# Kernel tuning notes

Measured on AMD Instinct MI355X. Metric: run time of the kernel, lower is better.

## Reference

```python
import jax, jax.numpy as jnp
import numpy as np

B, N, D, H = 8, 1024, 512, 8
DK = D // H  # key_dim == val_dim == 64
LN_EPS = 1e-5


def setup_inputs() -> dict:
    key = jax.random.key(0)
    ks = jax.random.split(key, 16)
    stdv = 1.0 / np.sqrt(D)
    u = lambda k, shape, s: jax.random.uniform(k, shape, jnp.float32, -s, s)
    inp = {
        'q': jax.random.normal(ks[0], (B, N, D), jnp.float32),
        'mask': jax.random.uniform(ks[1], (B, N, N)) < 0.1,  # True = masked out
        # eps1 is torch.zeros in the source (never re-initialized); use small
        'eps1': jax.random.normal(ks[2], (D, D), jnp.float32) * 0.03,
        # 3 MLP layers, stacked on leading axis. Linear: y = x @ W.T + b
        'U_w': u(ks[3], (3, D, D), stdv), 'U_b': u(ks[4], (3, D), stdv),
        'V_w': u(ks[5], (3, D, D), stdv), 'V_b': u(ks[6], (3, D), stdv),
        'ln_g': jnp.ones((3, D), jnp.float32), 'ln_b': jnp.zeros((3, D), jnp.float32),
        'W_query': u(ks[7], (H, D, DK), 1.0 / np.sqrt(DK)),
        'W_key':   u(ks[8], (H, D, DK), 1.0 / np.sqrt(DK)),
        'W_val':   u(ks[9], (H, D, DK), 1.0 / np.sqrt(DK)),
        'W_out':   u(ks[10], (H, DK, D), stdv),
    }
    return inp


def _layer_norm(x, g, b):
    mu = jnp.mean(x, axis=-1, keepdims=True)
    var = jnp.mean(jnp.square(x - mu), axis=-1, keepdims=True)
    return (x - mu) * jax.lax.rsqrt(var + LN_EPS) * g + b


def _mlp_layer(x, Uw, Ub, Vw, Vb, g, b):
    # U1 -> (identity maxpool k=1) -> V1 -> LayerNorm -> ReLU -> residual
    y = x @ Uw.T + Ub
    y = y @ Vw.T + Vb
    y = _layer_norm(y, g, b)
    return x + jax.nn.relu(y)


def reference(q, mask, eps1, U_w, U_b, V_w, V_b, ln_g, ln_b,
              W_query, W_key, W_val, W_out):
    nf = 1.0 / np.sqrt(DK)  # norm_factor; applied to BOTH Q and K as in source
    h = q
    for l in range(3):
        h = _mlp_layer(h @ eps1, U_w[l], U_b[l], V_w[l], V_b[l], ln_g[l], ln_b[l])
    # per-head projections: (H,B,N,DK)
    Q = jnp.einsum('bqd,hdk->hbqk', q, W_query) * nf
    K = jnp.einsum('bgd,hdk->hbgk', h, W_key) * nf
    V = jnp.einsum('bgd,hdk->hbgk', h, W_val)
    scores = jnp.einsum('hbqk,hbgk->hbqg', Q, K)  # (H,B,N,N)
    scores = jnp.where(mask[None], -1e10, scores)
    attn = jax.nn.softmax(scores, axis=-1)
    heads = jnp.einsum('hbqg,hbgv->hbqv', attn, V)
    out = jnp.einsum('hbqv,hvd->bqd', heads, W_out)  # (B,N,D)
    return out
```

## Files before the change

kernel.cpp:

```cpp
#include <hip/hip_runtime.h>

typedef __attribute__((ext_vector_type(8))) short bhalf8;
typedef __attribute__((ext_vector_type(4))) short bhalf4;
typedef __attribute__((ext_vector_type(4))) float f32x4;

__device__ __forceinline__ ushort f2bf(float f) {
  unsigned u = __builtin_bit_cast(unsigned, f);
  unsigned r = u + 0x7fffu + ((u >> 16) & 1u);
  return (ushort)(r >> 16);
}

__device__ __forceinline__ void gld16(const ushort* g, ushort* l) {
  __builtin_amdgcn_global_load_lds((const __attribute__((address_space(1))) void*)g,
                                   (__attribute__((address_space(3))) void*)l, 16, 0, 0);
}

__global__ __launch_bounds__(256) void prep_kernel(
    const float* __restrict__ q, const int* __restrict__ mask,
    const float* __restrict__ eps1, const float* __restrict__ U_w,
    const float* __restrict__ V_w, const float* __restrict__ Wq,
    const float* __restrict__ Wk, const float* __restrict__ Wv,
    const float* __restrict__ Wo, const float* __restrict__ U_b,
    const float* __restrict__ V_b,
    ushort* __restrict__ qb, unsigned long long* __restrict__ minv,
    ushort* __restrict__ uwb, ushort* __restrict__ vwb,
    ushort* __restrict__ e1b, ushort* __restrict__ e1t,
    ushort* __restrict__ wqkv, ushort* __restrict__ wot,
    float* __restrict__ cvec) {
  int i = blockIdx.x * 256 + threadIdx.x;
  if (i < 4194304) {
    qb[i] = f2bf(q[i]);
  } else if (i < 12582912) {
    int j = i - 4194304;
    unsigned long long bb = __ballot(mask[j] != 0);
    if ((threadIdx.x & 63) == 0) {
      int b = j >> 20, qq = (j >> 10) & 1023, g = j & 1023;
      minv[((size_t)b * 16 + (g >> 6)) * 1024 + qq] = ~bb;
    }
  } else if (i < 13369344) {
    int j = i - 12582912;
    uwb[j] = f2bf(U_w[j]);
  } else if (i < 14155776) {
    int j = i - 13369344;
    vwb[j] = f2bf(V_w[j]);
  } else if (i < 14417920) {
    int j = i - 14155776;
    e1b[j] = f2bf(eps1[j]);
  } else if (i < 14680064) {
    int j = i - 14417920; int n = j >> 9, k = j & 511;
    e1t[j] = f2bf(eps1[k * 512 + n]);
  } else if (i < 15466496) {
    int j = i - 14680064; int n = j >> 9, d = j & 511;
    const float* W = (n < 512) ? Wq : (n < 1024 ? Wk : Wv);
    float sc = (n < 512) ? 0.02255252509f : 1.0f;
    int nl = n & 511;
    wqkv[j] = f2bf(W[((nl >> 6) * 512 + d) * 64 + (nl & 63)] * sc);
  } else if (i < 15728640) {
    int j = i - 15466496; int d = j >> 9, hv = j & 511;
    wot[j] = f2bf(Wo[hv * 512 + d]);
  } else {
    int j = i - 15728640;
    int idx = j >> 6, ln = j & 63;
    int l = idx >> 9;
    const float* vr = V_w + (size_t)idx * 512 + ln * 8;
    const float* ur = U_b + l * 512 + ln * 8;
    float s = 0;
#pragma unroll
    for (int t = 0; t < 8; t++) s += vr[t] * ur[t];
#pragma unroll
    for (int off = 1; off < 64; off <<= 1) s += __shfl_xor(s, off, 64);
    if (ln == 0) cvec[idx] = s + V_b[idx];
  }
}

template <int BN>
__global__ __launch_bounds__(256) void gemm_nt(
    const ushort* __restrict__ A0, const ushort* __restrict__ A1,
    const ushort* __restrict__ Bt0, const ushort* __restrict__ Bt1,
    int bsplit, int mstride, int M, int K,
    ushort* __restrict__ Oa, const float* __restrict__ ba, int ca,
    ushort* __restrict__ Ob, const float* __restrict__ bb2, int cb,
    ushort* __restrict__ Oc, const float* __restrict__ bc, int cc) {
  __shared__ ushort As[128 * 32];
  __shared__ ushort Bs[BN * 32];
  int tid = threadIdx.x;
  int wave = tid >> 6, lane = tid & 63;
  int quad = lane >> 4, col = lane & 15;
  int m0 = blockIdx.x * 128, n0 = blockIdx.y * BN;
  const ushort* A = (A1 && n0 >= 512) ? A1 : A0;
  const ushort* Bp = ((n0 < bsplit) ? Bt0 + (size_t)n0 * K
                                    : Bt1 + (size_t)(n0 - bsplit) * K) +
                     (size_t)(m0 >> 9) * mstride;
  constexpr int NI = BN / 32;
  int wm = (BN == 128) ? (wave >> 1) * 64 : (wave & 1) * 64;
  int wn = (BN == 128) ? (wave & 1) * 64 : (wave >> 1) * 32;
  f32x4 acc[4][NI] = {};
  int srow = wave * 16 + (lane >> 2);
  int skc = (lane & 3) * 8;
  const ushort* gA0 = A + (size_t)(m0 + srow) * K + skc;
  const ushort* gA1 = gA0 + (size_t)64 * K;
  const ushort* gB0 = Bp + (size_t)srow * K + skc;
  const ushort* gB1 = gB0 + (size_t)64 * K;
  ushort* lA0 = &As[wave * 16 * 32];
  ushort* lA1 = &As[(64 + wave * 16) * 32];
  ushort* lB0 = &Bs[wave * 16 * 32];
  ushort* lB1 = (BN == 128) ? &Bs[(64 + wave * 16) * 32] : nullptr;

  gld16(gA0, lA0);
  gld16(gA1, lA1);
  gld16(gB0, lB0);
  if (BN == 128) gld16(gB1, lB1);

  for (int k0 = 0; k0 < K; k0 += 32) {
    __syncthreads();
    bhalf8 af[4], bg[NI];
#pragma unroll
    for (int i = 0; i < 4; i++)
      af[i] = *(bhalf8*)&As[(wm + i * 16 + col) * 32 + quad * 8];
#pragma unroll
    for (int i = 0; i < NI; i++)
      bg[i] = *(bhalf8*)&Bs[(wn + i * 16 + col) * 32 + quad * 8];
    __syncthreads();
    if (k0 + 32 < K) {
      gld16(gA0 + k0 + 32, lA0);
      gld16(gA1 + k0 + 32, lA1);
      gld16(gB0 + k0 + 32, lB0);
      if (BN == 128) gld16(gB1 + k0 + 32, lB1);
    }
#pragma unroll
    for (int mi = 0; mi < 4; mi++)
#pragma unroll
      for (int ni = 0; ni < NI; ni++)
        acc[mi][ni] = __builtin_amdgcn_mfma_f32_16x16x32_bf16(af[mi], bg[ni], acc[mi][ni], 0, 0, 0);
  }

  int reg = n0 >> 9;
  ushort* O = (reg == 0) ? Oa : (reg == 1 ? Ob : Oc);
  const float* bs = (reg == 0) ? ba : (reg == 1 ? bb2 : bc);
  int code = (reg == 0) ? ca : (reg == 1 ? cb : cc);
#pragma unroll
  for (int mi = 0; mi < 4; mi++)
#pragma unroll
    for (int ni = 0; ni < NI; ni++) {
      int cn = n0 + wn + ni * 16 + col;
      int cnl = cn & 511;
      int cmb = m0 + wm + mi * 16 + quad * 4;
      float bv = bs ? bs[cnl] : 0.f;
      if (code == 2) {
        int bhh = (cmb >> 10) * 8 + (cnl >> 6);
        size_t base = ((size_t)bhh * 64 + ((cmb & 1023) >> 4)) * 1024 +
                      (size_t)((cnl >> 5) & 1) * 512 + (size_t)(cmb & 15) * 32 + (cnl & 31);
#pragma unroll
        for (int r = 0; r < 4; r++)
          O[base + r * 32] = f2bf(acc[mi][ni][r] + bv);
      } else if (code == 3) {
        int bhh = (cmb >> 10) * 8 + (cnl >> 6);
        size_t base = ((size_t)bhh * 64 + ((cmb & 1023) >> 4)) * 1024 +
                      (size_t)(cnl & 63) * 16 + (cmb & 15);
        ushort4 pk;
        pk.x = f2bf(acc[mi][ni][0] + bv);
        pk.y = f2bf(acc[mi][ni][1] + bv);
        pk.z = f2bf(acc[mi][ni][2] + bv);
        pk.w = f2bf(acc[mi][ni][3] + bv);
        *(ushort4*)&O[base] = pk;
      } else if (code == 1) {
        float* Ff = (float*)O;
#pragma unroll
        for (int r = 0; r < 4; r++)
          Ff[(size_t)(cmb + r) * 512 + cnl] = acc[mi][ni][r] + bv;
      } else {
#pragma unroll
        for (int r = 0; r < 4; r++)
          O[(size_t)(cmb + r) * 512 + cnl] = f2bf(acc[mi][ni][r] + bv);
      }
    }
}

__global__ __launch_bounds__(256) void ln_kernel(
    const float* __restrict__ z, const ushort* __restrict__ tb,
    const float* __restrict__ lgam, const float* __restrict__ lbet,
    ushort* __restrict__ hb) {
  int row = blockIdx.x * 4 + (threadIdx.x >> 6);
  int lane = threadIdx.x & 63;
  int cbase = lane * 8;
  const float* zr = z + (size_t)row * 512 + cbase;
  float x[8];
  *(float4*)&x[0] = *(const float4*)zr;
  *(float4*)&x[4] = *(const float4*)(zr + 4);
  float sum = 0;
#pragma unroll
  for (int i = 0; i < 8; i++) sum += x[i];
#pragma unroll
  for (int off = 1; off < 64; off <<= 1) sum += __shfl_xor(sum, off, 64);
  float mu = sum * (1.f / 512.f);
  float vs = 0;
#pragma unroll
  for (int i = 0; i < 8; i++) { float d = x[i] - mu; vs += d * d; }
#pragma unroll
  for (int off = 1; off < 64; off <<= 1) vs += __shfl_xor(vs, off, 64);
  float rstd = rsqrtf(vs * (1.f / 512.f) + 1e-5f);
  uint4 tr = *(const uint4*)&tb[(size_t)row * 512 + cbase];
  float tv[8];
  {
    const unsigned* u = (const unsigned*)&tr;
#pragma unroll
    for (int w = 0; w < 4; w++) {
      tv[2 * w] = __builtin_bit_cast(float, u[w] << 16);
      tv[2 * w + 1] = __builtin_bit_cast(float, u[w] & 0xFFFF0000u);
    }
  }
  ushort outv[8];
#pragma unroll
  for (int i = 0; i < 8; i++) {
    float val = (x[i] - mu) * rstd * lgam[cbase + i] + lbet[cbase + i];
    outv[i] = f2bf(tv[i] + fmaxf(val, 0.f));
  }
  *(uint4*)&hb[(size_t)row * 512 + cbase] = *(uint4*)outv;
}

__global__ __launch_bounds__(256, 3) void attn_kernel(
    const ushort* __restrict__ QtT, const ushort* __restrict__ KtT,
    const ushort* __restrict__ VtT, const unsigned long long* __restrict__ minv,
    ushort* __restrict__ Op) {
  int bh = blockIdx.x, qt0 = blockIdx.y;
  int b = bh >> 3, h = bh & 7;
  __shared__ float R[64 * 68];
  int tid = threadIdx.x, w = tid >> 6, lane = tid & 63;
  int quad = lane >> 4, col = lane & 15;
  int q0 = qt0 * 64;
  const ushort* Kt = KtT + (size_t)bh * 65536 + col * 32 + quad * 8;
  const ushort* Vt = VtT + (size_t)bh * 65536 + col * 16 + quad * 4;
  const ushort* Qt = QtT + (size_t)bh * 65536 + col * 32 + quad * 8;
  bhalf8 bq[4][2];
#pragma unroll
  for (int qt = 0; qt < 4; qt++)
#pragma unroll
    for (int ks = 0; ks < 2; ks++)
      bq[qt][ks] = *(const bhalf8*)(Qt + (size_t)(qt0 * 4 + qt) * 1024 + ks * 512);
  f32x4 o[4][4] = {};
  float lsum[4] = {0.f, 0.f, 0.f, 0.f};
  const unsigned long long* mb = minv + (size_t)b * 16384 + q0 + col;

  for (int g0 = 0; g0 < 1024; g0 += 128) {
    int gs = g0 + w * 32;
    int gw = gs >> 6;
    int sb = (gs & 32) + quad * 4;
    unsigned shq[4];
#pragma unroll
    for (int qt = 0; qt < 4; qt++)
      shq[qt] = (unsigned)(mb[gw * 1024 + qt * 16] >> sb);
#pragma unroll
    for (int gt = 0; gt < 2; gt++) {
      size_t gblk = (size_t)((gs >> 4) + gt) * 1024;
      bhalf8 ak0 = *(const bhalf8*)(Kt + gblk);
      bhalf8 ak1 = *(const bhalf8*)(Kt + gblk + 512);
      bhalf4 av[4];
#pragma unroll
      for (int vt = 0; vt < 4; vt++)
        av[vt] = *(const bhalf4*)(Vt + gblk + vt * 256);
#pragma unroll
      for (int qt = 0; qt < 4; qt++) {
        f32x4 s = {};
        s = __builtin_amdgcn_mfma_f32_16x16x32_bf16(ak0, bq[qt][0], s, 0, 0, 0);
        s = __builtin_amdgcn_mfma_f32_16x16x32_bf16(ak1, bq[qt][1], s, 0, 0, 0);
        unsigned sh = shq[qt];
        unsigned pu[4];
#pragma unroll
        for (int r = 0; r < 4; r++) {
          const int pos = gt * 16 + r;
          unsigned keep = (unsigned)((int)(sh << (31 - pos)) >> 31);
          pu[r] = __builtin_bit_cast(unsigned, __builtin_amdgcn_exp2f(s[r])) & keep;
          lsum[qt] += __builtin_bit_cast(float, pu[r]);
        }
        uint2 pp;
        pp.x = ((pu[0] + 0x8000u) >> 16) | (((pu[1] + 0x8000u) >> 16) << 16);
        pp.y = ((pu[2] + 0x8000u) >> 16) | (((pu[3] + 0x8000u) >> 16) << 16);
        bhalf4 bp = __builtin_bit_cast(bhalf4, pp);
#pragma unroll
        for (int vt = 0; vt < 4; vt++)
          o[vt][qt] = __builtin_amdgcn_mfma_f32_16x16x16bf16_1k(av[vt], bp, o[vt][qt], 0, 0, 0);
      }
    }
  }
  for (int src = 1; src < 4; src++) {
    __syncthreads();
    if (w == src) {
      float* dst = R + lane * 68;
#pragma unroll
      for (int vt = 0; vt < 4; vt++)
#pragma unroll
        for (int qt = 0; qt < 4; qt++)
          *(f32x4*)(dst + (vt * 4 + qt) * 4) = o[vt][qt];
#pragma unroll
      for (int qt = 0; qt < 4; qt++) dst[64 + qt] = lsum[qt];
    }
    __syncthreads();
    if (w == 0) {
      const float* sp = R + lane * 68;
#pragma unroll
      for (int vt = 0; vt < 4; vt++)
#pragma unroll
        for (int qt = 0; qt < 4; qt++)
          o[vt][qt] += *(const f32x4*)(sp + (vt * 4 + qt) * 4);
#pragma unroll
      for (int qt = 0; qt < 4; qt++) lsum[qt] += sp[64 + qt];
    }
  }
  if (w == 0) {
    float rl[4];
#pragma unroll
    for (int qt = 0; qt < 4; qt++) {
      lsum[qt] += __shfl_xor(lsum[qt], 16, 64);
      lsum[qt] += __shfl_xor(lsum[qt], 32, 64);
      rl[qt] = __builtin_amdgcn_rcpf(lsum[qt]);
    }
#pragma unroll
    for (int vt = 0; vt < 4; vt++)
#pragma unroll
      for (int qt = 0; qt < 4; qt++) {
        ushort4 pk;
        pk.x = f2bf(o[vt][qt][0] * rl[qt]);
        pk.y = f2bf(o[vt][qt][1] * rl[qt]);
        pk.z = f2bf(o[vt][qt][2] * rl[qt]);
        pk.w = f2bf(o[vt][qt][3] * rl[qt]);
        *(ushort4*)&Op[(size_t)(b * 1024 + q0 + qt * 16 + col) * 512 +
                       h * 64 + vt * 16 + quad * 4] = pk;
      }
  }
}

extern "C" void kernel_launch(void* const* d_in, const int* in_sizes, int n_in,
                              void* d_out, int out_size, void* d_ws, size_t ws_size,
                              hipStream_t stream) {
  const float* q    = (const float*)d_in[0];
  const int*   mask = (const int*)d_in[1];
  const float* eps1 = (const float*)d_in[2];
  const float* U_w  = (const float*)d_in[3];
  const float* U_b  = (const float*)d_in[4];
  const float* V_w  = (const float*)d_in[5];
  const float* V_b  = (const float*)d_in[6];
  const float* ln_g = (const float*)d_in[7];
  const float* ln_b = (const float*)d_in[8];
  const float* Wq   = (const float*)d_in[9];
  const float* Wk   = (const float*)d_in[10];
  const float* Wv   = (const float*)d_in[11];
  const float* Wo   = (const float*)d_in[12];
  float* out = (float*)d_out;

  char* ws = (char*)d_ws;
  auto carve = [&](size_t bytes) { char* p = ws; ws += bytes; return p; };
  ushort* qb   = (ushort*)carve(8388608);
  ushort* uwb  = (ushort*)carve(1572864);
  ushort* vwb  = (ushort*)carve(1572864);
  ushort* e1b  = (ushort*)carve(524288);
  ushort* e1t  = (ushort*)carve(524288);
  ushort* wqkv = (ushort*)carve(1572864);
  ushort* wot  = (ushort*)carve(524288);
  ushort* A1b  = (ushort*)carve(1572864);
  ushort* Gtb  = (ushort*)carve(1572864);
  float*  cvec = (float*)carve(6144);
  unsigned long long* minv = (unsigned long long*)carve(1048576);
  ushort* tb   = (ushort*)carve(8388608);
  float*  zf   = (float*)carve(16777216);
  ushort* hb   = (ushort*)carve(8388608);
  ushort* Qtt  = (ushort*)carve(8388608);
  ushort* Ktt  = (ushort*)carve(8388608);
  ushort* Vtt  = (ushort*)carve(8388608);
  ushort* Ob   = (ushort*)carve(8388608);
  const int BIG = 1 << 30;

  prep_kernel<<<61824, 256, 0, stream>>>(q, mask, eps1, U_w, V_w, Wq, Wk, Wv, Wo,
                                         U_b, V_b, qb, minv, uwb, vwb, e1b, e1t,
                                         wqkv, wot, cvec);
  gemm_nt<128><<<dim3(4, 12), 256, 0, stream>>>(
      e1b, nullptr, uwb, nullptr, BIG, 0, 512, 512,
      A1b, nullptr, 0, A1b + 262144, nullptr, 0, A1b + 524288, nullptr, 0);
  gemm_nt<64><<<dim3(12, 8), 256, 0, stream>>>(
      vwb, nullptr, A1b, nullptr, BIG, 262144, 1536, 512,
      Gtb, nullptr, 0, nullptr, nullptr, 0, nullptr, nullptr, 0);
  const ushort* hsrc = qb;
  for (int l = 0; l < 3; l++) {
    gemm_nt<128><<<dim3(64, 8), 256, 0, stream>>>(
        hsrc, nullptr, e1t, Gtb + l * 262144, 512, 0, 8192, 512,
        tb, nullptr, 0, (ushort*)zf, cvec + l * 512, 1, nullptr, nullptr, 0);
    ln_kernel<<<2048, 256, 0, stream>>>(zf, tb, ln_g + l * 512, ln_b + l * 512, hb);
    hsrc = hb;
  }
  gemm_nt<128><<<dim3(64, 12), 256, 0, stream>>>(
      qb, hb, wqkv, nullptr, BIG, 0, 8192, 512,
      Qtt, nullptr, 2, Ktt, nullptr, 2, Vtt, nullptr, 3);
  attn_kernel<<<dim3(64, 16), 256, 0, stream>>>(Qtt, Ktt, Vtt, minv, Ob);
  gemm_nt<64><<<dim3(64, 8), 256, 0, stream>>>(
      Ob, nullptr, wot, nullptr, BIG, 0, 8192, 512,
      (ushort*)out, nullptr, 1, nullptr, nullptr, 0, nullptr, nullptr, 0);
}
```

Before: 305.4 us.

## Give each wave its own query tile and double-buffer K/V register loads

The attention kernel now assigns each wave a separate 16-query tile that walks the full key range. Previously the four waves split the key range for a shared 64-query block and then reduced their partial outputs through shared memory with repeated barriers. Removing that reduction also frees the LDS buffer and the syncthreads calls. K/V fragments are prefetched into two alternating register sets so loads overlap the MFMA work, and occupancy is raised to 4 blocks per CU. In exchange, every wave now reads the full K/V stream for its head, so per-wave K/V global/L2 traffic grows fourfold.

```diff
diff --git a/kernel.cpp b/kernel.cpp
--- a/kernel.cpp
+++ b/kernel.cpp
@@ -218,114 +218,89 @@
   *(uint4*)&hb[(size_t)row * 512 + cbase] = *(uint4*)outv;
 }
 
-__global__ __launch_bounds__(256, 3) void attn_kernel(
+struct KVb { bhalf8 k[4]; bhalf4 v[8]; };
+
+__device__ __forceinline__ void ldkv(KVb& d, const ushort* kp, const ushort* vp) {
+  d.k[0] = *(const bhalf8*)kp;
+  d.k[1] = *(const bhalf8*)(kp + 512);
+  d.k[2] = *(const bhalf8*)(kp + 1024);
+  d.k[3] = *(const bhalf8*)(kp + 1536);
+#pragma unroll
+  for (int i = 0; i < 8; i++) d.v[i] = *(const bhalf4*)(vp + i * 256);
+}
+
+__device__ __forceinline__ void attn_step(const KVb& kv, unsigned long long m,
+                                          int bs, int quad, bhalf8 bq0, bhalf8 bq1,
+                                          f32x4* o, float& lsum) {
+  unsigned shq = (unsigned)(m >> (bs + quad * 4));
+#pragma unroll
+  for (int gt = 0; gt < 2; ++gt) {
+    f32x4 s = {};
+    s = __builtin_amdgcn_mfma_f32_16x16x32_bf16(kv.k[2 * gt], bq0, s, 0, 0, 0);
+    s = __builtin_amdgcn_mfma_f32_16x16x32_bf16(kv.k[2 * gt + 1], bq1, s, 0, 0, 0);
+    unsigned pu[4];
+#pragma unroll
+    for (int r = 0; r < 4; ++r) {
+      const int pos = gt * 16 + r;
+      unsigned keep = (unsigned)((int)(shq << (31 - pos)) >> 31);
+      pu[r] = __builtin_bit_cast(unsigned, __builtin_amdgcn_exp2f(s[r])) & keep;
+      lsum += __builtin_bit_cast(float, pu[r]);
+    }
+    uint2 pp;
+    pp.x = ((pu[0] + 0x8000u) >> 16) | (((pu[1] + 0x8000u) >> 16) << 16);
+    pp.y = ((pu[2] + 0x8000u) >> 16) | (((pu[3] + 0x8000u) >> 16) << 16);
+    bhalf4 bp = __builtin_bit_cast(bhalf4, pp);
+#pragma unroll
+    for (int vt = 0; vt < 4; ++vt)
+      o[vt] = __builtin_amdgcn_mfma_f32_16x16x16bf16_1k(kv.v[gt * 4 + vt], bp, o[vt], 0, 0, 0);
+  }
+}
+
+__global__ __launch_bounds__(256, 4) void attn_kernel(
     const ushort* __restrict__ QtT, const ushort* __restrict__ KtT,
     const ushort* __restrict__ VtT, const unsigned long long* __restrict__ minv,
     ushort* __restrict__ Op) {
-  int bh = blockIdx.x, qt0 = blockIdx.y;
+  int bh = blockIdx.x;
   int b = bh >> 3, h = bh & 7;
-  __shared__ float R[64 * 68];
   int tid = threadIdx.x, w = tid >> 6, lane = tid & 63;
   int quad = lane >> 4, col = lane & 15;
-  int q0 = qt0 * 64;
+  int qt = blockIdx.y * 4 + w;
   const ushort* Kt = KtT + (size_t)bh * 65536 + col * 32 + quad * 8;
   const ushort* Vt = VtT + (size_t)bh * 65536 + col * 16 + quad * 4;
   const ushort* Qt = QtT + (size_t)bh * 65536 + col * 32 + quad * 8;
-  bhalf8 bq[4][2];
-#pragma unroll
-  for (int qt = 0; qt < 4; qt++)
-#pragma unroll
-    for (int ks = 0; ks < 2; ks++)
-      bq[qt][ks] = *(const bhalf8*)(Qt + (size_t)(qt0 * 4 + qt) * 1024 + ks * 512);
-  f32x4 o[4][4] = {};
-  float lsum[4] = {0.f, 0.f, 0.f, 0.f};
-  const unsigned long long* mb = minv + (size_t)b * 16384 + q0 + col;
-
-  for (int g0 = 0; g0 < 1024; g0 += 128) {
-    int gs = g0 + w * 32;
-    int gw = gs >> 6;
-    int sb = (gs & 32) + quad * 4;
-    unsigned shq[4];
-#pragma unroll
-    for (int qt = 0; qt < 4; qt++)
-      shq[qt] = (unsigned)(mb[gw * 1024 + qt * 16] >> sb);
-#pragma unroll
-    for (int gt = 0; gt < 2; gt++) {
-      size_t gblk = (size_t)((gs >> 4) + gt) * 1024;
-      bhalf8 ak0 = *(const bhalf8*)(Kt + gblk);
-      bhalf8 ak1 = *(const bhalf8*)(Kt + gblk + 512);
-      bhalf4 av[4];
-#pragma unroll
-      for (int vt = 0; vt < 4; vt++)
-        av[vt] = *(const bhalf4*)(Vt + gblk + vt * 256);
-#pragma unroll
-      for (int qt = 0; qt < 4; qt++) {
-        f32x4 s = {};
-        s = __builtin_amdgcn_mfma_f32_16x16x32_bf16(ak0, bq[qt][0], s, 0, 0, 0);
-        s = __builtin_amdgcn_mfma_f32_16x16x32_bf16(ak1, bq[qt][1], s, 0, 0, 0);
-        unsigned sh = shq[qt];
-        unsigned pu[4];
-#pragma unroll
-        for (int r = 0; r < 4; r++) {
-          const int pos = gt * 16 + r;
-          unsigned keep = (unsigned)((int)(sh << (31 - pos)) >> 31);
-          pu[r] = __builtin_bit_cast(unsigned, __builtin_amdgcn_exp2f(s[r])) & keep;
-          lsum[qt] += __builtin_bit_cast(float, pu[r]);
-        }
-        uint2 pp;
-        pp.x = ((pu[0] + 0x8000u) >> 16) | (((pu[1] + 0x8000u) >> 16) << 16);
-        pp.y = ((pu[2] + 0x8000u) >> 16) | (((pu[3] + 0x8000u) >> 16) << 16);
-        bhalf4 bp = __builtin_bit_cast(bhalf4, pp);
-#pragma unroll
-        for (int vt = 0; vt < 4; vt++)
-          o[vt][qt] = __builtin_amdgcn_mfma_f32_16x16x16bf16_1k(av[vt], bp, o[vt][qt], 0, 0, 0);
-      }
-    }
-  }
-  for (int src = 1; src < 4; src++) {
-    __syncthreads();
-    if (w == src) {
-      float* dst = R + lane * 68;
-#pragma unroll
-      for (int vt = 0; vt < 4; vt++)
-#pragma unroll
-        for (int qt = 0; qt < 4; qt++)
-          *(f32x4*)(dst + (vt * 4 + qt) * 4) = o[vt][qt];
-#pragma unroll
-      for (int qt = 0; qt < 4; qt++) dst[64 + qt] = lsum[qt];
-    }
-    __syncthreads();
-    if (w == 0) {
-      const float* sp = R + lane * 68;
-#pragma unroll
-      for (int vt = 0; vt < 4; vt++)
-#pragma unroll
-        for (int qt = 0; qt < 4; qt++)
-          o[vt][qt] += *(const f32x4*)(sp + (vt * 4 + qt) * 4);
-#pragma unroll
-      for (int qt = 0; qt < 4; qt++) lsum[qt] += sp[64 + qt];
-    }
-  }
-  if (w == 0) {
-    float rl[4];
-#pragma unroll
-    for (int qt = 0; qt < 4; qt++) {
-      lsum[qt] += __shfl_xor(lsum[qt], 16, 64);
-      lsum[qt] += __shfl_xor(lsum[qt], 32, 64);
-      rl[qt] = __builtin_amdgcn_rcpf(lsum[qt]);
-    }
-#pragma unroll
-    for (int vt = 0; vt < 4; vt++)
-#pragma unroll
-      for (int qt = 0; qt < 4; qt++) {
-        ushort4 pk;
-        pk.x = f2bf(o[vt][qt][0] * rl[qt]);
-        pk.y = f2bf(o[vt][qt][1] * rl[qt]);
-        pk.z = f2bf(o[vt][qt][2] * rl[qt]);
-        pk.w = f2bf(o[vt][qt][3] * rl[qt]);
-        *(ushort4*)&Op[(size_t)(b * 1024 + q0 + qt * 16 + col) * 512 +
-                       h * 64 + vt * 16 + quad * 4] = pk;
-      }
+  bhalf8 bq0 = *(const bhalf8*)(Qt + (size_t)qt * 1024);
+  bhalf8 bq1 = *(const bhalf8*)(Qt + (size_t)qt * 1024 + 512);
+  f32x4 o[4] = {};
+  float lsum = 0.f;
+  const unsigned long long* mb = minv + (size_t)b * 16384 + qt * 16 + col;
+
+  KVb A, Bv;
+  unsigned long long mcur = mb[0], mnxt = 0;
+  ldkv(A, Kt, Vt);
+  for (int p = 0; p < 30; p += 2) {
+    ldkv(Bv, Kt + (size_t)(p + 1) * 2048, Vt + (size_t)(p + 1) * 2048);
+    mnxt = mb[((p >> 1) + 1) * 1024];
+    attn_step(A, mcur, 0, quad, bq0, bq1, o, lsum);
+    ldkv(A, Kt + (size_t)(p + 2) * 2048, Vt + (size_t)(p + 2) * 2048);
+    attn_step(Bv, mcur, 32, quad, bq0, bq1, o, lsum);
+    mcur = mnxt;
+  }
+  ldkv(Bv, Kt + (size_t)31 * 2048, Vt + (size_t)31 * 2048);
+  attn_step(A, mcur, 0, quad, bq0, bq1, o, lsum);
+  attn_step(Bv, mcur, 32, quad, bq0, bq1, o, lsum);
+
+  lsum += __shfl_xor(lsum, 16, 64);
+  lsum += __shfl_xor(lsum, 32, 64);
+  float rl = __builtin_amdgcn_rcpf(lsum);
+  int q = qt * 16 + col;
+#pragma unroll
+  for (int vt = 0; vt < 4; ++vt) {
+    ushort4 pk;
+    pk.x = f2bf(o[vt][0] * rl);
+    pk.y = f2bf(o[vt][1] * rl);
+    pk.z = f2bf(o[vt][2] * rl);
+    pk.w = f2bf(o[vt][3] * rl);
+    *(ushort4*)&Op[(size_t)(b * 1024 + q) * 512 + h * 64 + vt * 16 + quad * 4] = pk;
   }
 }
 
```

Result: slower. 332.4 us (+8.9%).
